# Performance work log

Hardware: AMD Instinct MI355X
Metric: run time of the kernel (lower is better)

## Reference

```python
import jax, jax.numpy as jnp
import numpy as np

HID = 1024
NH = 16
DH = HID // NH  # 64


def _heads(x):
    # [B, S, H] -> [B, nH, S, dh]
    B, S, _ = x.shape
    return x.reshape(B, S, NH, DH).transpose(0, 2, 1, 3)


def setup_inputs() -> dict:
    key = jax.random.key(0)
    ks = jax.random.split(key, 16)
    inp = {
        "word_hidden_states": jax.random.normal(ks[0], (2, 2048, HID), jnp.float32),
        "entity_hidden_states": jax.random.normal(ks[1], (2, 256, HID), jnp.float32),
    }
    scale = 1.0 / np.sqrt(HID)
    names = ["Wq", "Wk", "Wv", "Ww2e", "We2w", "We2e"]
    for i, n in enumerate(names):
        inp[n] = jax.random.normal(ks[2 + i], (HID, HID), jnp.float32) * scale
        inp["b" + n[1:]] = jnp.zeros((HID,), jnp.float32)
    return inp


def reference(word_hidden_states, entity_hidden_states,
              Wq, bq, Wk, bk, Wv, bv,
              Ww2e, bw2e, We2w, be2w, We2e, be2e):
    word, ent = word_hidden_states, entity_hidden_states
    B, Sw, _ = word.shape
    Se = ent.shape[1]
    hs = jnp.concatenate([word, ent], axis=1)  # [B, Sw+Se, H]

    # four query types, heads: [B, nH, S*, dh]
    q_w2w = _heads(word @ Wq + bq)
    q_w2e = _heads(word @ Ww2e + bw2e)
    q_e2w = _heads(ent @ We2w + be2w)
    q_e2e = _heads(ent @ We2e + be2e)

    k = _heads(hs @ Wk + bk)
    v = _heads(hs @ Wv + bv)
    k_w, k_e = k[:, :, :Sw, :], k[:, :, Sw:, :]

    # block scores
    s_w2w = jnp.einsum("bhqd,bhkd->bhqk", q_w2w, k_w)  # [B,nH,Sw,Sw]
    s_w2e = jnp.einsum("bhqd,bhkd->bhqk", q_w2e, k_e)  # [B,nH,Sw,Se]
    s_e2w = jnp.einsum("bhqd,bhkd->bhqk", q_e2w, k_w)  # [B,nH,Se,Sw]
    s_e2e = jnp.einsum("bhqd,bhkd->bhqk", q_e2e, k_e)  # [B,nH,Se,Se]

    word_scores = jnp.concatenate([s_w2w, s_w2e], axis=3)
    ent_scores = jnp.concatenate([s_e2w, s_e2e], axis=3)
    scores = jnp.concatenate([word_scores, ent_scores], axis=2)  # [B,nH,S,S]
    scores = scores / np.sqrt(DH)

    probs = jax.nn.softmax(scores, axis=-1)  # dropout is identity in eval
    ctx = jnp.einsum("bhqk,bhkd->bhqd", probs, v)  # [B,nH,S,dh]
    ctx = ctx.transpose(0, 2, 1, 3).reshape(B, Sw + Se, HID)
    return ctx[:, :Sw, :], ctx[:, Sw:, :]
```

## Files before the change

kernel.cpp:

```cpp
#include <hip/hip_runtime.h>
#include <hip/hip_bf16.h>

typedef __attribute__((ext_vector_type(8))) short short8;
typedef __attribute__((ext_vector_type(4))) float f32x4;
typedef __attribute__((ext_vector_type(16))) float f32x16;
typedef __attribute__((ext_vector_type(4))) unsigned short u16x4;
typedef __attribute__((ext_vector_type(8))) unsigned short u16x8;
typedef __attribute__((ext_vector_type(4))) unsigned int u32x4;

__device__ __forceinline__ unsigned short f2b(float f) {
  __hip_bfloat16 h = __float2bfloat16(f);
  return __builtin_bit_cast(unsigned short, h);
}

__device__ __forceinline__ void gload_lds16(const void* g, void* l) {
  __builtin_amdgcn_global_load_lds(
      (const __attribute__((address_space(1))) unsigned int*)g,
      (__attribute__((address_space(3))) unsigned int*)l, 16, 0, 0);
}

__device__ __forceinline__ f32x16 mfma32(short8 a, short8 b, f32x16 c) {
  return __builtin_amdgcn_mfma_f32_32x32x16_bf16(a, b, c, 0, 0, 0);
}

__device__ __forceinline__ unsigned int cvtpk(float a, float b) {
  unsigned int r;
  asm("v_cvt_pk_bf16_f32 %0, %1, %2" : "=v"(r) : "v"(a), "v"(b));
  return r;
}

__global__ __launch_bounds__(256) void cvt_all(const float* __restrict__ sw,
                                               const float* __restrict__ se,
                                               unsigned short* __restrict__ dw,
                                               unsigned short* __restrict__ de) {
  int i = blockIdx.x * 256 + threadIdx.x;
  const float* s;
  unsigned short* d;
  int j;
  if (i < 524288) {
    s = sw; d = dw; j = i;
  } else {
    s = se; d = de; j = i - 524288;
    if (j >= 65536) return;
  }
  const f32x4* sp = (const f32x4*)s;
  f32x4 a = sp[2 * j];
  f32x4 b = sp[2 * j + 1];
  u16x8 o;
  o[0] = f2b(a[0]); o[1] = f2b(a[1]); o[2] = f2b(a[2]); o[3] = f2b(a[3]);
  o[4] = f2b(b[0]); o[5] = f2b(b[1]); o[6] = f2b(b[2]); o[7] = f2b(b[3]);
  ((u16x8*)d)[j] = o;
}

struct WtransParams {
  const float* w[6];
  unsigned short* wt[6];
};

__global__ __launch_bounds__(256) void wtrans(WtransParams p) {
  __shared__ float t[32][33];
  const int z = blockIdx.z;
  const float* W = p.w[z];
  unsigned short* Wt = p.wt[z];
  const int bx = blockIdx.x;
  const int by = blockIdx.y;
  const int tx = threadIdx.x, ty = threadIdx.y;
#pragma unroll
  for (int i = 0; i < 4; ++i)
    t[ty + 8 * i][tx] = W[(by * 32 + ty + 8 * i) * 1024 + bx * 32 + tx];
  __syncthreads();
#pragma unroll
  for (int i = 0; i < 4; ++i)
    Wt[(bx * 32 + ty + 8 * i) * 1024 + by * 32 + tx] = f2b(t[tx][ty + 8 * i]);
}

struct GemmJob {
  const unsigned short* Wt;
  const float* bias;
  unsigned short* out;
  int S;
  int s_off;
  int sshift;
  int trans;
  float scale;
};
struct Gemm2Params {
  const unsigned short* Aw;
  const unsigned short* Ae;
  GemmJob job[8];
};

__global__ __launch_bounds__(256) void gemm_qkv(Gemm2Params p) {
  __shared__ unsigned short As[128 * 64];
  __shared__ unsigned short Bs[128 * 64];
  const int tid = threadIdx.x;
  const int w = tid >> 6, lane = tid & 63;
  const int c = lane & 15, g = lane >> 4;
  const int z = blockIdx.z;
  const int y = blockIdx.y;
  const bool isw = y < 32;
  const GemmJob j = p.job[isw ? z : z + 4];
  const unsigned short* A = isw ? p.Aw : p.Ae;
  const long arow0 = (long)(isw ? y : y - 32) * 128;
  const unsigned short* B = j.Wt;
  const long brow0 = (long)blockIdx.x * 128;

  f32x4 acc[4][4] = {};

  for (int kt = 0; kt < 16; ++kt) {
    __syncthreads();
#pragma unroll
    for (int i = 0; i < 4; ++i) {
      int ch = i * 256 + tid;
      int row = ch >> 3;
      int k8 = ((ch & 7) ^ (row & 7)) << 3;
      const unsigned short* ga = A + (arow0 + row) * 1024 + kt * 64 + k8;
      const unsigned short* gb = B + (brow0 + row) * 1024 + kt * 64 + k8;
      gload_lds16(ga, As + (i * 256 + w * 64) * 8);
      gload_lds16(gb, Bs + (i * 256 + w * 64) * 8);
    }
    __syncthreads();
#pragma unroll
    for (int kf = 0; kf < 2; ++kf) {
      short8 av[4], bv[4];
#pragma unroll
      for (int mf = 0; mf < 4; ++mf) {
        int row = (w >> 1) * 64 + mf * 16 + c;
        int byte = (row * 128 + (kf * 32 + g * 8) * 2) ^ ((row & 7) << 4);
        av[mf] = *(const short8*)((const char*)As + byte);
      }
#pragma unroll
      for (int nf = 0; nf < 4; ++nf) {
        int row = (w & 1) * 64 + nf * 16 + c;
        int byte = (row * 128 + (kf * 32 + g * 8) * 2) ^ ((row & 7) << 4);
        bv[nf] = *(const short8*)((const char*)Bs + byte);
      }
      __builtin_amdgcn_s_setprio(1);
#pragma unroll
      for (int mf = 0; mf < 4; ++mf)
#pragma unroll
        for (int nf = 0; nf < 4; ++nf)
          acc[mf][nf] = __builtin_amdgcn_mfma_f32_16x16x32_bf16(av[mf], bv[nf],
                                                                acc[mf][nf], 0, 0, 0);
      __builtin_amdgcn_s_setprio(0);
    }
  }

  float biasv[4];
#pragma unroll
  for (int nf = 0; nf < 4; ++nf) {
    int n = (int)brow0 + (w & 1) * 64 + nf * 16 + c;
    biasv[nf] = j.bias[n];
  }
  const int smask = (1 << j.sshift) - 1;
  if (j.trans) {
#pragma unroll
    for (int mf = 0; mf < 4; ++mf) {
      int m0 = (int)arow0 + (w >> 1) * 64 + mf * 16 + g * 4;
      int b_ = m0 >> j.sshift;
      int s = (m0 & smask) + j.s_off;
#pragma unroll
      for (int nf = 0; nf < 4; ++nf) {
        int n = (int)brow0 + (w & 1) * 64 + nf * 16 + c;
        int hh = n >> 6, dd = n & 63;
        u16x4 pv;
#pragma unroll
        for (int r = 0; r < 4; ++r)
          pv[r] = f2b((acc[mf][nf][r] + biasv[nf]) * j.scale);
        *(u16x4*)(j.out + (((long)b_ * 16 + hh) * 64 + dd) * 2304 + s) = pv;
      }
    }
  } else {
#pragma unroll
    for (int mf = 0; mf < 4; ++mf) {
#pragma unroll
      for (int r = 0; r < 4; ++r) {
        int m = (int)arow0 + (w >> 1) * 64 + mf * 16 + g * 4 + r;
        int b_ = m >> j.sshift;
        int s = (m & smask) + j.s_off;
#pragma unroll
        for (int nf = 0; nf < 4; ++nf) {
          int n = (int)brow0 + (w & 1) * 64 + nf * 16 + c;
          int hh = n >> 6, dd = n & 63;
          float v = (acc[mf][nf][r] + biasv[nf]) * j.scale;
          j.out[(((long)b_ * 16 + hh) * j.S + s) * 64 + dd] = f2b(v);
        }
      }
    }
  }
}

__global__ __launch_bounds__(256, 2) void attn_kernel(
    const unsigned short* __restrict__ qw2w, const unsigned short* __restrict__ qw2e,
    const unsigned short* __restrict__ qe2w, const unsigned short* __restrict__ qe2e,
    const unsigned short* __restrict__ Kg, const unsigned short* __restrict__ Vtg,
    float* __restrict__ out) {
  __shared__ unsigned short smem[33280];

  const int tid = threadIdx.x;
  const int w = tid >> 6, lane = tid & 63;
  const int l31 = lane & 31, hf = lane >> 5;

  const int flat = blockIdx.x;
  const int work = (flat & 7) * 144 + (flat >> 3);
  const int tile = work % 36;
  const int hb = work / 36;
  const int head = hb & 15, b = hb >> 4;

  const bool isw = tile < 32;
  const int Sq = isw ? 2048 : 256;
  const int q0 = (isw ? tile : tile - 32) * 64;
  const int bh = b * 16 + head;
  const unsigned short* Qa =
      (isw ? qw2w : qe2w) + ((long)bh * Sq + q0 + l31) * 64 + hf * 8;
  const unsigned short* Qb =
      (isw ? qw2e : qe2e) + ((long)bh * Sq + q0 + l31) * 64 + hf * 8;
  const unsigned short* Kb = Kg + (long)bh * 2304 * 64;
  const unsigned short* Vtb = Vtg + (long)bh * 64 * 2304;

  short8 qcur[2][4];
#pragma unroll
  for (int qh = 0; qh < 2; ++qh)
#pragma unroll
    for (int kf = 0; kf < 4; ++kf)
      qcur[qh][kf] = *(const short8*)(Qa + qh * 2048 + kf * 16);

  f32x16 o[2][2] = {};
  float lrun[2] = {0.f, 0.f};

  auto stage = [&](int t, int bufi) {
    unsigned short* kb = smem + w * 8192 + bufi * 4096;
    unsigned short* vb = kb + 2048;
    const int key0s = w * 576 + t * 32;
#pragma unroll
    for (int i = 0; i < 4; ++i) {
      int c = i * 64 + lane;
      int row = c >> 3, slot = c & 7;
      int sl = slot ^ (row & 7);
      gload_lds16(Kb + (key0s + row) * 64 + sl * 8, kb + i * 512);
      int d = row + ((sl >> 2) << 5);
      int k8 = (sl & 3) << 3;
      gload_lds16(Vtb + (long)d * 2304 + key0s + k8, vb + i * 512);
    }
  };

  stage(0, 0);
  int cur = 0;
  const int swz = (l31 & 7) << 4;

  for (int t = 0; t < 18; ++t) {
    if (w * 576 + t * 32 == 2048) {
#pragma unroll
      for (int qh = 0; qh < 2; ++qh)
#pragma unroll
        for (int kf = 0; kf < 4; ++kf)
          qcur[qh][kf] = *(const short8*)(Qb + qh * 2048 + kf * 16);
    }
    if (t < 17) {
      stage(t + 1, cur ^ 1);
      asm volatile("s_waitcnt vmcnt(8)" ::: "memory");
    } else {
      asm volatile("s_waitcnt vmcnt(0)" ::: "memory");
    }
    __builtin_amdgcn_sched_barrier(0);

    const char* KbaseC = (const char*)(smem + w * 8192 + cur * 4096);
    const char* VbaseC = KbaseC + 4096;

    short8 kfr[4];
#pragma unroll
    for (int kf = 0; kf < 4; ++kf)
      kfr[kf] = *(const short8*)(KbaseC + l31 * 128 + (((kf * 32) | (hf * 16)) ^ swz));
    f32x16 st0 = {}, st1 = {};
    __builtin_amdgcn_s_setprio(1);
#pragma unroll
    for (int kf = 0; kf < 4; ++kf) {
      st0 = mfma32(kfr[kf], qcur[0][kf], st0);
      st1 = mfma32(kfr[kf], qcur[1][kf], st1);
    }
    __builtin_amdgcn_s_setprio(0);

    float s0 = 0.f, s1 = 0.f, s2 = 0.f, s3 = 0.f;
    float u0 = 0.f, u1 = 0.f, u2 = 0.f, u3 = 0.f;
#pragma unroll
    for (int r = 0; r < 16; r += 4) {
      float p0 = __builtin_amdgcn_exp2f(st0[r + 0]);
      float p1 = __builtin_amdgcn_exp2f(st0[r + 1]);
      float p2 = __builtin_amdgcn_exp2f(st0[r + 2]);
      float p3 = __builtin_amdgcn_exp2f(st0[r + 3]);
      st0[r + 0] = p0; st0[r + 1] = p1; st0[r + 2] = p2; st0[r + 3] = p3;
      s0 += p0; s1 += p1; s2 += p2; s3 += p3;
      float q0_ = __builtin_amdgcn_exp2f(st1[r + 0]);
      float q1_ = __builtin_amdgcn_exp2f(st1[r + 1]);
      float q2_ = __builtin_amdgcn_exp2f(st1[r + 2]);
      float q3_ = __builtin_amdgcn_exp2f(st1[r + 3]);
      st1[r + 0] = q0_; st1[r + 1] = q1_; st1[r + 2] = q2_; st1[r + 3] = q3_;
      u0 += q0_; u1 += q1_; u2 += q2_; u3 += q3_;
    }
    lrun[0] += (s0 + s1) + (s2 + s3);
    lrun[1] += (u0 + u1) + (u2 + u3);

#pragma unroll
    for (int hs = 0; hs < 2; ++hs) {
      const int rbase = hs * 8;
      unsigned int a0 = cvtpk(st0[rbase + 0], st0[rbase + 1]);
      unsigned int a1 = cvtpk(st0[rbase + 2], st0[rbase + 3]);
      unsigned int b0 = cvtpk(st0[rbase + 4], st0[rbase + 5]);
      unsigned int b1 = cvtpk(st0[rbase + 6], st0[rbase + 7]);
      asm("v_permlane32_swap_b32 %0, %1" : "+v"(a0), "+v"(b0));
      asm("v_permlane32_swap_b32 %0, %1" : "+v"(a1), "+v"(b1));
      u32x4 pw0;
      pw0[0] = a0; pw0[1] = a1; pw0[2] = b0; pw0[3] = b1;
      short8 pf0 = __builtin_bit_cast(short8, pw0);
      unsigned int c0 = cvtpk(st1[rbase + 0], st1[rbase + 1]);
      unsigned int c1 = cvtpk(st1[rbase + 2], st1[rbase + 3]);
      unsigned int d0 = cvtpk(st1[rbase + 4], st1[rbase + 5]);
      unsigned int d1 = cvtpk(st1[rbase + 6], st1[rbase + 7]);
      asm("v_permlane32_swap_b32 %0, %1" : "+v"(c0), "+v"(d0));
      asm("v_permlane32_swap_b32 %0, %1" : "+v"(c1), "+v"(d1));
      u32x4 pw1;
      pw1[0] = c0; pw1[1] = c1; pw1[2] = d0; pw1[3] = d1;
      short8 pf1 = __builtin_bit_cast(short8, pw1);
      short8 vf0 = *(const short8*)(VbaseC + l31 * 128 +
                                    (((hs * 2 + hf) ^ (l31 & 7)) << 4));
      short8 vf1 = *(const short8*)(VbaseC + l31 * 128 +
                                    (((4 + hs * 2 + hf) ^ (l31 & 7)) << 4));
      __builtin_amdgcn_s_setprio(1);
      o[0][0] = mfma32(vf0, pf0, o[0][0]);
      o[0][1] = mfma32(vf1, pf0, o[0][1]);
      o[1][0] = mfma32(vf0, pf1, o[1][0]);
      o[1][1] = mfma32(vf1, pf1, o[1][1]);
      __builtin_amdgcn_s_setprio(0);
    }

    cur ^= 1;
  }

  float lt0 = lrun[0] + __shfl_xor(lrun[0], 32);
  float lt1 = lrun[1] + __shfl_xor(lrun[1], 32);
  float* Lf = (float*)(smem + 32768);
  if (lane < 32) {
    Lf[w * 64 + lane] = lt0;
    Lf[w * 64 + 32 + lane] = lt1;
  }
#pragma unroll
  for (int qh = 0; qh < 2; ++qh)
#pragma unroll
    for (int mf = 0; mf < 2; ++mf)
#pragma unroll
      for (int rg = 0; rg < 4; ++rg) {
        int q = qh * 32 + l31;
        int d4 = mf * 8 + rg * 2 + hf;
        f32x4 v;
        v[0] = o[qh][mf][rg * 4 + 0];
        v[1] = o[qh][mf][rg * 4 + 1];
        v[2] = o[qh][mf][rg * 4 + 2];
        v[3] = o[qh][mf][rg * 4 + 3];
        *(f32x4*)((char*)smem + w * 16384 + q * 256 + ((d4 ^ (q & 7)) << 4)) = v;
      }
  __syncthreads();

  float* ob = isw ? out + (((long)b * 2048 + q0) * 1024 + head * 64)
                  : out + 4194304 + (((long)b * 256 + q0) * 1024 + head * 64);
  const int q = tid >> 2;
  float inv = 1.f / (Lf[q] + Lf[64 + q] + Lf[128 + q] + Lf[192 + q]);
#pragma unroll
  for (int i = 0; i < 4; ++i) {
    int c = (tid & 3) * 4 + i;
    f32x4 s = {};
#pragma unroll
    for (int ww = 0; ww < 4; ++ww) {
      f32x4 pv = *(const f32x4*)((const char*)smem + ww * 16384 + q * 256 +
                                 ((c ^ (q & 7)) << 4));
      s += pv;
    }
    s *= inv;
    *(f32x4*)(ob + (long)q * 1024 + c * 4) = s;
  }
}

extern "C" void kernel_launch(void* const* d_in, const int* in_sizes, int n_in,
                              void* d_out, int out_size, void* d_ws, size_t ws_size,
                              hipStream_t stream) {
  (void)in_sizes; (void)n_in; (void)out_size; (void)ws_size;
  const float* word = (const float*)d_in[0];
  const float* ent = (const float*)d_in[1];

  char* ws = (char*)d_ws;
  size_t off = 0;
  auto alloc = [&](size_t bytes) {
    void* p = ws + off;
    off += (bytes + 255) & ~(size_t)255;
    return p;
  };
  unsigned short* Xw = (unsigned short*)alloc(4096ull * 1024 * 2);
  unsigned short* Xe = (unsigned short*)alloc(512ull * 1024 * 2);
  unsigned short* Wt[6];
  for (int i = 0; i < 6; ++i) Wt[i] = (unsigned short*)alloc(1024ull * 1024 * 2);
  unsigned short* qw2w = (unsigned short*)alloc(2ull * 16 * 2048 * 64 * 2);
  unsigned short* qw2e = (unsigned short*)alloc(2ull * 16 * 2048 * 64 * 2);
  unsigned short* qe2w = (unsigned short*)alloc(2ull * 16 * 256 * 64 * 2);
  unsigned short* qe2e = (unsigned short*)alloc(2ull * 16 * 256 * 64 * 2);
  unsigned short* Kbuf = (unsigned short*)alloc(2ull * 16 * 2304 * 64 * 2);
  unsigned short* Vtbuf = (unsigned short*)alloc(2ull * 16 * 64 * 2304 * 2);

  cvt_all<<<2304, 256, 0, stream>>>(word, ent, Xw, Xe);

  WtransParams wp;
  wp.w[0] = (const float*)d_in[2];
  wp.w[1] = (const float*)d_in[4];
  wp.w[2] = (const float*)d_in[6];
  wp.w[3] = (const float*)d_in[8];
  wp.w[4] = (const float*)d_in[10];
  wp.w[5] = (const float*)d_in[12];
  for (int i = 0; i < 6; ++i) wp.wt[i] = Wt[i];
  wtrans<<<dim3(32, 32, 6), dim3(32, 8), 0, stream>>>(wp);

  const float* bq = (const float*)d_in[3];
  const float* bk = (const float*)d_in[5];
  const float* bv = (const float*)d_in[7];
  const float* bw2e = (const float*)d_in[9];
  const float* be2w = (const float*)d_in[11];
  const float* be2e = (const float*)d_in[13];
  const float qs = 0.125f * 1.44269504f;

  Gemm2Params gp;
  gp.Aw = Xw;
  gp.Ae = Xe;
  gp.job[0] = {Wt[0], bq, qw2w, 2048, 0, 11, 0, qs};
  gp.job[1] = {Wt[3], bw2e, qw2e, 2048, 0, 11, 0, qs};
  gp.job[2] = {Wt[1], bk, Kbuf, 2304, 0, 11, 0, 1.f};
  gp.job[3] = {Wt[2], bv, Vtbuf, 2304, 0, 11, 1, 1.f};
  gp.job[4] = {Wt[4], be2w, qe2w, 256, 0, 8, 0, qs};
  gp.job[5] = {Wt[5], be2e, qe2e, 256, 0, 8, 0, qs};
  gp.job[6] = {Wt[1], bk, Kbuf, 2304, 2048, 8, 0, 1.f};
  gp.job[7] = {Wt[2], bv, Vtbuf, 2304, 2048, 8, 1, 1.f};
  gemm_qkv<<<dim3(8, 36, 4), 256, 0, stream>>>(gp);

  attn_kernel<<<1152, 256, 0, stream>>>(qw2w, qw2e, qe2w, qe2e, Kbuf, Vtbuf,
                                        (float*)d_out);
}
```

Before: 149.1 us.

## Single-buffer K/V staging and halve LDS to raise attention occupancy

Replaces the double-buffered per-wave K/V LDS staging with a single buffer. All K and V fragments are read into registers up front, then the next tile's async global-to-LDS load is issued during compute. The epilogue reduction is split into two halves so it fits the smaller LDS footprint. LDS usage drops to about half and launch bounds go from 2 to 4 blocks per CU, aiming for more waves in flight to hide latency. The cost is a full vmcnt(0) wait each iteration, less in-block overlap of loads, and extra registers held for V fragments.

```diff
diff --git a/kernel.cpp b/kernel.cpp
--- a/kernel.cpp
+++ b/kernel.cpp
@@ -190,12 +190,12 @@
   }
 }
 
-__global__ __launch_bounds__(256, 2) void attn_kernel(
+__global__ __launch_bounds__(256, 4) void attn_kernel(
     const unsigned short* __restrict__ qw2w, const unsigned short* __restrict__ qw2e,
     const unsigned short* __restrict__ qe2w, const unsigned short* __restrict__ qe2e,
     const unsigned short* __restrict__ Kg, const unsigned short* __restrict__ Vtg,
     float* __restrict__ out) {
-  __shared__ unsigned short smem[33280];
+  __shared__ unsigned short smem[16896];
 
   const int tid = threadIdx.x;
   const int w = tid >> 6, lane = tid & 63;
@@ -228,8 +228,8 @@
   f32x16 o[2][2] = {};
   float lrun[2] = {0.f, 0.f};
 
-  auto stage = [&](int t, int bufi) {
-    unsigned short* kb = smem + w * 8192 + bufi * 4096;
+  auto stage = [&](int t) {
+    unsigned short* kb = smem + w * 4096;
     unsigned short* vb = kb + 2048;
     const int key0s = w * 576 + t * 32;
 #pragma unroll
@@ -244,9 +244,10 @@
     }
   };
 
-  stage(0, 0);
-  int cur = 0;
+  stage(0);
   const int swz = (l31 & 7) << 4;
+  const char* KbaseC = (const char*)(smem + w * 4096);
+  const char* VbaseC = KbaseC + 4096;
 
   for (int t = 0; t < 18; ++t) {
     if (w * 576 + t * 32 == 2048) {
@@ -256,21 +257,24 @@
         for (int kf = 0; kf < 4; ++kf)
           qcur[qh][kf] = *(const short8*)(Qb + qh * 2048 + kf * 16);
     }
-    if (t < 17) {
-      stage(t + 1, cur ^ 1);
-      asm volatile("s_waitcnt vmcnt(8)" ::: "memory");
-    } else {
-      asm volatile("s_waitcnt vmcnt(0)" ::: "memory");
-    }
+
+    asm volatile("s_waitcnt vmcnt(0)" ::: "memory");
     __builtin_amdgcn_sched_barrier(0);
-
-    const char* KbaseC = (const char*)(smem + w * 8192 + cur * 4096);
-    const char* VbaseC = KbaseC + 4096;
-
-    short8 kfr[4];
+    short8 kfr[4], vfr[2][2];
 #pragma unroll
     for (int kf = 0; kf < 4; ++kf)
       kfr[kf] = *(const short8*)(KbaseC + l31 * 128 + (((kf * 32) | (hf * 16)) ^ swz));
+#pragma unroll
+    for (int hs = 0; hs < 2; ++hs) {
+      vfr[hs][0] = *(const short8*)(VbaseC + l31 * 128 +
+                                    (((hs * 2 + hf) ^ (l31 & 7)) << 4));
+      vfr[hs][1] = *(const short8*)(VbaseC + l31 * 128 +
+                                    (((4 + hs * 2 + hf) ^ (l31 & 7)) << 4));
+    }
+    asm volatile("s_waitcnt lgkmcnt(0)" ::: "memory");
+    __builtin_amdgcn_sched_barrier(0);
+    if (t < 17) stage(t + 1);
+
     f32x16 st0 = {}, st1 = {};
     __builtin_amdgcn_s_setprio(1);
 #pragma unroll
@@ -321,61 +325,59 @@
       u32x4 pw1;
       pw1[0] = c0; pw1[1] = c1; pw1[2] = d0; pw1[3] = d1;
       short8 pf1 = __builtin_bit_cast(short8, pw1);
-      short8 vf0 = *(const short8*)(VbaseC + l31 * 128 +
-                                    (((hs * 2 + hf) ^ (l31 & 7)) << 4));
-      short8 vf1 = *(const short8*)(VbaseC + l31 * 128 +
-                                    (((4 + hs * 2 + hf) ^ (l31 & 7)) << 4));
       __builtin_amdgcn_s_setprio(1);
-      o[0][0] = mfma32(vf0, pf0, o[0][0]);
-      o[0][1] = mfma32(vf1, pf0, o[0][1]);
-      o[1][0] = mfma32(vf0, pf1, o[1][0]);
-      o[1][1] = mfma32(vf1, pf1, o[1][1]);
+      o[0][0] = mfma32(vfr[hs][0], pf0, o[0][0]);
+      o[0][1] = mfma32(vfr[hs][1], pf0, o[0][1]);
+      o[1][0] = mfma32(vfr[hs][0], pf1, o[1][0]);
+      o[1][1] = mfma32(vfr[hs][1], pf1, o[1][1]);
       __builtin_amdgcn_s_setprio(0);
     }
-
-    cur ^= 1;
   }
 
   float lt0 = lrun[0] + __shfl_xor(lrun[0], 32);
   float lt1 = lrun[1] + __shfl_xor(lrun[1], 32);
-  float* Lf = (float*)(smem + 32768);
+  float* Lf = (float*)(smem + 16384);
   if (lane < 32) {
     Lf[w * 64 + lane] = lt0;
     Lf[w * 64 + 32 + lane] = lt1;
   }
-#pragma unroll
-  for (int qh = 0; qh < 2; ++qh)
+
+  float* ob = isw ? out + (((long)b * 2048 + q0) * 1024 + head * 64)
+                  : out + 4194304 + (((long)b * 256 + q0) * 1024 + head * 64);
+
+#pragma unroll
+  for (int qh = 0; qh < 2; ++qh) {
+    __syncthreads();
 #pragma unroll
     for (int mf = 0; mf < 2; ++mf)
 #pragma unroll
       for (int rg = 0; rg < 4; ++rg) {
-        int q = qh * 32 + l31;
         int d4 = mf * 8 + rg * 2 + hf;
         f32x4 v;
         v[0] = o[qh][mf][rg * 4 + 0];
         v[1] = o[qh][mf][rg * 4 + 1];
         v[2] = o[qh][mf][rg * 4 + 2];
         v[3] = o[qh][mf][rg * 4 + 3];
-        *(f32x4*)((char*)smem + w * 16384 + q * 256 + ((d4 ^ (q & 7)) << 4)) = v;
-      }
-  __syncthreads();
-
-  float* ob = isw ? out + (((long)b * 2048 + q0) * 1024 + head * 64)
-                  : out + 4194304 + (((long)b * 256 + q0) * 1024 + head * 64);
-  const int q = tid >> 2;
-  float inv = 1.f / (Lf[q] + Lf[64 + q] + Lf[128 + q] + Lf[192 + q]);
-#pragma unroll
-  for (int i = 0; i < 4; ++i) {
-    int c = (tid & 3) * 4 + i;
-    f32x4 s = {};
-#pragma unroll
-    for (int ww = 0; ww < 4; ++ww) {
-      f32x4 pv = *(const f32x4*)((const char*)smem + ww * 16384 + q * 256 +
-                                 ((c ^ (q & 7)) << 4));
-      s += pv;
-    }
-    s *= inv;
-    *(f32x4*)(ob + (long)q * 1024 + c * 4) = s;
+        *(f32x4*)((char*)smem + w * 8192 + l31 * 256 + ((d4 ^ (l31 & 7)) << 4)) = v;
+      }
+    __syncthreads();
+    const int row = tid >> 3;
+    const int cbase = (tid & 7) * 2;
+    float inv = 1.f / (Lf[qh * 32 + row] + Lf[64 + qh * 32 + row] +
+                       Lf[128 + qh * 32 + row] + Lf[192 + qh * 32 + row]);
+#pragma unroll
+    for (int i = 0; i < 2; ++i) {
+      int c = cbase + i;
+      f32x4 s = {};
+#pragma unroll
+      for (int ww = 0; ww < 4; ++ww) {
+        f32x4 pv = *(const f32x4*)((const char*)smem + ww * 8192 + row * 256 +
+                                   ((c ^ (row & 7)) << 4));
+        s += pv;
+      }
+      s *= inv;
+      *(f32x4*)(ob + (long)(qh * 32 + row) * 1024 + c * 4) = s;
+    }
   }
 }
 
```

New measurement: 535.0 us. 259% more time.
